# Optimization experiments

Hardware: AMD Instinct MI355X
Metric: run time of the kernel (lower is better)

The kernel has to match this reference:

```python
import jax, jax.numpy as jnp
import numpy as np

A, V, T = 32, 32, 128          # per-modality hidden dims
PF = 128                       # post_fusion_dim
FUSED = (A + 1) * (V + 1) * (T + 1)  # 140481
B = 256


def setup_inputs() -> dict:
    key = jax.random.key(0)
    ks = jax.random.split(key, 9)
    s1 = 1.0 / np.sqrt(FUSED)
    s2 = 1.0 / np.sqrt(PF)
    return {
        "audio_x": jax.random.normal(ks[0], (B, A), dtype=jnp.float32),
        "video_x": jax.random.normal(ks[1], (B, V), dtype=jnp.float32),
        "text_x": jax.random.normal(ks[2], (B, T), dtype=jnp.float32),
        "W1": jax.random.uniform(ks[3], (FUSED, PF), jnp.float32, -s1, s1),
        "b1": jax.random.uniform(ks[4], (PF,), jnp.float32, -s1, s1),
        "W2": jax.random.uniform(ks[5], (PF, PF), jnp.float32, -s2, s2),
        "b2": jax.random.uniform(ks[6], (PF,), jnp.float32, -s2, s2),
        "W3": jax.random.uniform(ks[7], (PF, 1), jnp.float32, -s2, s2),
        "b3": jax.random.uniform(ks[8], (1,), jnp.float32, -s2, s2),
    }


def reference(audio_x, video_x, text_x, W1, b1, W2, b2, W3, b3):
    b = audio_x.shape[0]
    ones = jnp.ones((b, 1), dtype=audio_x.dtype)
    a = jnp.concatenate([ones, audio_x], axis=1)  # (B, A+1)
    v = jnp.concatenate([ones, video_x], axis=1)  # (B, V+1)
    t = jnp.concatenate([ones, text_x], axis=1)   # (B, T+1)
    # trilinear outer product, flattened: (B, (A+1)*(V+1)*(T+1))
    fusion = jnp.einsum("ba,bv,bt->bavt", a, v, t).reshape(b, -1)
    h1 = jax.nn.relu(fusion @ W1 + b1)
    h2 = jax.nn.relu(h1 @ W2 + b2)
    return h2 @ W3 + b3
```

## Files before the change

kernel.cpp:

```cpp
#include <hip/hip_runtime.h>
#include <hip/hip_bf16.h>
#include <stdint.h>

#define BATCH 256
#define PFD 128
#define T1 129
#define NPAIRS 1089
#define BKSTR 72
#define CHUNK 8

typedef short bf16x8 __attribute__((ext_vector_type(8)));
typedef float f32x4 __attribute__((ext_vector_type(4)));

static __device__ __forceinline__ unsigned bits_of(float f){ union{float f;unsigned u;}x;x.f=f;return x.u; }
static __device__ __forceinline__ float float_of(unsigned u){ union{float f;unsigned u;}x;x.u=u;return x.f; }
static __device__ __forceinline__ unsigned pk_bf16(float a, float b){
  union { __hip_bfloat162 h; unsigned u; } c;
  c.h = __float22bfloat162_rn(make_float2(a, b));
  return c.u;
}

__global__ __launch_bounds__(512, 2) void tfn_k1(
    const float* __restrict__ audio, const float* __restrict__ video,
    const float* __restrict__ text, const float* __restrict__ W1,
    unsigned short* __restrict__ part, int S) {
  __shared__ __align__(16) short b_lds[2][PFD * BKSTR];
  __shared__ __align__(16) float av_lds[BATCH * CHUNK];

  const int tid = threadIdx.x;
  const int bk = blockIdx.x;
  const int npb = NPAIRS / S, rem0 = NPAIRS % S;
  const int p0 = bk * npb + (bk < rem0 ? bk : rem0);
  const int np = npb + (bk < rem0 ? 1 : 0);

  const int wave = tid >> 6, lane = tid & 63;
  const int l15 = lane & 15, quad = lane >> 4;
  const int sn = tid & 127, skg = tid >> 7;

  float treg[2][32];
  float t128r[2];
  #pragma unroll
  for (int mt = 0; mt < 2; ++mt) {
    const int m = wave * 32 + mt * 16 + l15;
    t128r[mt] = text[m * 128 + 127];
    #pragma unroll
    for (int ks = 0; ks < 4; ++ks)
      #pragma unroll
      for (int j = 0; j < 8; ++j) {
        const int it = ks * 32 + quad * 8 + j;
        treg[mt][ks * 8 + j] = (it == 0) ? 1.0f : text[m * 128 + it - 1];
      }
  }

  f32x4 acc[2][8];
  #pragma unroll
  for (int a = 0; a < 2; ++a)
    #pragma unroll
    for (int b = 0; b < 8; ++b) acc[a][b] = f32x4{0.f, 0.f, 0.f, 0.f};

  float pf0[16], pf1[16], rv[8];

  for (int c0 = 0; c0 < np; c0 += CHUNK) {
    const int nc = (np - c0) < CHUNK ? (np - c0) : CHUNK;
    const int pbase = p0 + c0;
    __syncthreads();
    if (tid < BATCH) {
      const int m = tid;
      for (int j = 0; j < nc; ++j) {
        int p = pbase + j;
        int ia = p / 33, iv = p - ia * 33;
        float a = (ia == 0) ? 1.0f : audio[m * 32 + ia - 1];
        float v = (iv == 0) ? 1.0f : video[m * 32 + iv - 1];
        av_lds[m * CHUNK + j] = a * v;
      }
    }
    #pragma unroll
    for (int j = 0; j < 8; ++j) {
      int kk = skg * 8 + j;
      rv[j] = (kk < nc) ? W1[((long)(pbase + kk) * T1 + 128) * PFD + sn] : 0.0f;
    }
    {
      const long rb = (long)pbase * T1;
      #pragma unroll
      for (int g = 0; g < 2; ++g)
        #pragma unroll
        for (int j = 0; j < 8; ++j) {
          pf0[g * 8 + j] = W1[(rb + g * 32 + skg * 8 + j) * PFD + sn];
          pf1[g * 8 + j] = W1[(rb + 64 + g * 32 + skg * 8 + j) * PFD + sn];
        }
    }
    for (int sp = 0; sp < nc; ++sp) {
      float avm[2];
      __syncthreads();
      avm[0] = av_lds[(wave * 32 + l15) * CHUNK + sp];
      avm[1] = av_lds[(wave * 32 + 16 + l15) * CHUNK + sp];
      {
        union { bf16x8 v; unsigned u[4]; } w0, w1;
        #pragma unroll
        for (int d = 0; d < 4; ++d) {
          w0.u[d] = pk_bf16(pf0[2 * d], pf0[2 * d + 1]);
          w1.u[d] = pk_bf16(pf0[8 + 2 * d], pf0[8 + 2 * d + 1]);
        }
        *(bf16x8*)&b_lds[0][sn * BKSTR + skg * 8] = w0.v;
        *(bf16x8*)&b_lds[0][sn * BKSTR + 32 + skg * 8] = w1.v;
      }
      if (sp + 1 < nc) {
        const long rb = (long)(pbase + sp + 1) * T1;
        #pragma unroll
        for (int g = 0; g < 2; ++g)
          #pragma unroll
          for (int j = 0; j < 8; ++j)
            pf0[g * 8 + j] = W1[(rb + g * 32 + skg * 8 + j) * PFD + sn];
      }
      __syncthreads();
      #pragma unroll
      for (int ks = 0; ks < 2; ++ks) {
        bf16x8 A0, A1;
        {
          union { bf16x8 v; unsigned u[4]; } c0u, c1u;
          #pragma unroll
          for (int d = 0; d < 4; ++d) {
            c0u.u[d] = pk_bf16(avm[0] * treg[0][ks * 8 + 2 * d], avm[0] * treg[0][ks * 8 + 2 * d + 1]);
            c1u.u[d] = pk_bf16(avm[1] * treg[1][ks * 8 + 2 * d], avm[1] * treg[1][ks * 8 + 2 * d + 1]);
          }
          A0 = c0u.v; A1 = c1u.v;
        }
        #pragma unroll
        for (int nt = 0; nt < 8; ++nt) {
          bf16x8 bf = *(const bf16x8*)&b_lds[0][(nt * 16 + l15) * BKSTR + ks * 32 + quad * 8];
          acc[0][nt] = __builtin_amdgcn_mfma_f32_16x16x32_bf16(A0, bf, acc[0][nt], 0, 0, 0);
          acc[1][nt] = __builtin_amdgcn_mfma_f32_16x16x32_bf16(A1, bf, acc[1][nt], 0, 0, 0);
        }
      }
      __syncthreads();
      {
        union { bf16x8 v; unsigned u[4]; } w0, w1;
        #pragma unroll
        for (int d = 0; d < 4; ++d) {
          w0.u[d] = pk_bf16(pf1[2 * d], pf1[2 * d + 1]);
          w1.u[d] = pk_bf16(pf1[8 + 2 * d], pf1[8 + 2 * d + 1]);
        }
        *(bf16x8*)&b_lds[1][sn * BKSTR + skg * 8] = w0.v;
        *(bf16x8*)&b_lds[1][sn * BKSTR + 32 + skg * 8] = w1.v;
      }
      if (sp + 1 < nc) {
        const long rb = (long)(pbase + sp + 1) * T1 + 64;
        #pragma unroll
        for (int g = 0; g < 2; ++g)
          #pragma unroll
          for (int j = 0; j < 8; ++j)
            pf1[g * 8 + j] = W1[(rb + g * 32 + skg * 8 + j) * PFD + sn];
      }
      __syncthreads();
      #pragma unroll
      for (int ks2 = 0; ks2 < 2; ++ks2) {
        const int ks = 2 + ks2;
        bf16x8 A0, A1;
        {
          union { bf16x8 v; unsigned u[4]; } c0u, c1u;
          #pragma unroll
          for (int d = 0; d < 4; ++d) {
            c0u.u[d] = pk_bf16(avm[0] * treg[0][ks * 8 + 2 * d], avm[0] * treg[0][ks * 8 + 2 * d + 1]);
            c1u.u[d] = pk_bf16(avm[1] * treg[1][ks * 8 + 2 * d], avm[1] * treg[1][ks * 8 + 2 * d + 1]);
          }
          A0 = c0u.v; A1 = c1u.v;
        }
        #pragma unroll
        for (int nt = 0; nt < 8; ++nt) {
          bf16x8 bf = *(const bf16x8*)&b_lds[1][(nt * 16 + l15) * BKSTR + ks2 * 32 + quad * 8];
          acc[0][nt] = __builtin_amdgcn_mfma_f32_16x16x32_bf16(A0, bf, acc[0][nt], 0, 0, 0);
          acc[1][nt] = __builtin_amdgcn_mfma_f32_16x16x32_bf16(A1, bf, acc[1][nt], 0, 0, 0);
        }
      }
    }
    __syncthreads();
    {
      union { bf16x8 v; unsigned u[4]; } w;
      #pragma unroll
      for (int d = 0; d < 4; ++d) w.u[d] = pk_bf16(rv[2 * d], rv[2 * d + 1]);
      *(bf16x8*)&b_lds[0][sn * BKSTR + skg * 8] = w.v;
    }
    __syncthreads();
    {
      bf16x8 A[2];
      #pragma unroll
      for (int mt = 0; mt < 2; ++mt) {
        const int m = wave * 32 + mt * 16 + l15;
        union { bf16x8 v; unsigned u[4]; } c;
        #pragma unroll
        for (int d = 0; d < 4; ++d) {
          int k0 = quad * 8 + 2 * d, k1 = k0 + 1;
          float f0 = (k0 < nc) ? av_lds[m * CHUNK + k0] * t128r[mt] : 0.0f;
          float f1 = (k1 < nc) ? av_lds[m * CHUNK + k1] * t128r[mt] : 0.0f;
          c.u[d] = pk_bf16(f0, f1);
        }
        A[mt] = c.v;
      }
      #pragma unroll
      for (int nt = 0; nt < 8; ++nt) {
        bf16x8 bf = *(const bf16x8*)&b_lds[0][(nt * 16 + l15) * BKSTR + quad * 8];
        acc[0][nt] = __builtin_amdgcn_mfma_f32_16x16x32_bf16(A[0], bf, acc[0][nt], 0, 0, 0);
        acc[1][nt] = __builtin_amdgcn_mfma_f32_16x16x32_bf16(A[1], bf, acc[1][nt], 0, 0, 0);
      }
    }
  }

  #pragma unroll
  for (int mt = 0; mt < 2; ++mt)
    #pragma unroll
    for (int r = 0; r < 4; ++r) {
      const int m = wave * 32 + mt * 16 + quad * 4 + r;
      union { bf16x8 v; unsigned u[4]; } w;
      #pragma unroll
      for (int d = 0; d < 4; ++d) w.u[d] = pk_bf16(acc[mt][2 * d][r], acc[mt][2 * d + 1][r]);
      *(bf16x8*)&part[((size_t)m * S + bk) * PFD + l15 * 8] = w.v;
    }
}

__global__ __launch_bounds__(1024) void tfn_k2(
    const unsigned short* __restrict__ part, const float* __restrict__ b1,
    const float* __restrict__ W2, const float* __restrict__ b2,
    const float* __restrict__ W3, const float* __restrict__ b3,
    float* __restrict__ out, int S) {
  __shared__ float sred[1024 * 4];
  __shared__ float h1s[PFD];
  __shared__ float a2s[1024];
  __shared__ float red[2];
  const int m = blockIdx.x, tid = threadIdx.x;
  const int g = tid & 31, q = tid >> 5;
  const unsigned short* base = part + (size_t)m * S * PFD;
  float s0 = 0, s1 = 0, s2 = 0, s3 = 0;
  for (int bkk = q; bkk < S; bkk += 32) {
    uint2 v = *(const uint2*)&base[(size_t)bkk * PFD + g * 4];
    s0 += float_of(v.x << 16);
    s1 += float_of(v.x & 0xFFFF0000u);
    s2 += float_of(v.y << 16);
    s3 += float_of(v.y & 0xFFFF0000u);
  }
  sred[tid * 4 + 0] = s0; sred[tid * 4 + 1] = s1;
  sred[tid * 4 + 2] = s2; sred[tid * 4 + 3] = s3;
  __syncthreads();
  if (tid < PFD) {
    const int p = tid;
    float h = 0;
    #pragma unroll
    for (int bl = 0; bl < 32; ++bl) h += sred[(bl * 32 + (p >> 2)) * 4 + (p & 3)];
    const int n = (p & 7) * 16 + (p >> 3);
    h1s[n] = fmaxf(h + b1[n], 0.0f);
  }
  __syncthreads();
  const int n = tid & 127, kq = tid >> 7;
  float a2 = 0.0f;
  const int k0 = kq * 16;
  #pragma unroll
  for (int k = 0; k < 16; ++k) a2 += h1s[k0 + k] * W2[(k0 + k) * PFD + n];
  a2s[tid] = a2;
  __syncthreads();
  if (tid < 128) {
    float h2 = 0.0f;
    #pragma unroll
    for (int j = 0; j < 8; ++j) h2 += a2s[n + 128 * j];
    h2 = fmaxf(h2 + b2[n], 0.0f);
    float pr = h2 * W3[n];
    #pragma unroll
    for (int off = 32; off > 0; off >>= 1) pr += __shfl_down(pr, off);
    if ((tid & 63) == 0) red[tid >> 6] = pr;
  }
  __syncthreads();
  if (tid == 0) out[m] = red[0] + red[1] + b3[0];
}

extern "C" void kernel_launch(void* const* d_in, const int* in_sizes, int n_in,
                              void* d_out, int out_size, void* d_ws, size_t ws_size,
                              hipStream_t stream) {
  const float* audio = (const float*)d_in[0];
  const float* video = (const float*)d_in[1];
  const float* text  = (const float*)d_in[2];
  const float* W1 = (const float*)d_in[3];
  const float* b1 = (const float*)d_in[4];
  const float* W2 = (const float*)d_in[5];
  const float* b2 = (const float*)d_in[6];
  const float* W3 = (const float*)d_in[7];
  const float* b3 = (const float*)d_in[8];
  unsigned short* part = (unsigned short*)d_ws;

  const size_t slab = (size_t)BATCH * PFD * sizeof(unsigned short);
  int S = (int)(ws_size / slab);
  if (S > 512) S = 512;
  if (S < 1) S = 1;

  tfn_k1<<<S, 512, 0, stream>>>(audio, video, text, W1, part, S);
  tfn_k2<<<BATCH, 1024, 0, stream>>>(part, b1, W2, b2, W3, b3, (float*)d_out, S);
}
```

Measured before the change: 145.3 us.

## Stage full K tile per pair in double-buffered LDS and cap grid at 256

The per-pair loop used to stage W1 in two 64-row halves, each with its own pair of barriers. It now converts all 128 rows of a pair into one of two LDS buffers chosen by pair parity. That cuts the barriers to one per pair and lets the next pair's global prefetch overlap the MFMA work. The LDS row stride grows to fit the full tile, which raises shared memory per block. The number of split-K blocks is also capped at 256 instead of 512, which shrinks the partial sums the second kernel must reduce but gives each block more pairs and fewer blocks per CU.

```diff
diff --git a/kernel.cpp b/kernel.cpp
--- a/kernel.cpp
+++ b/kernel.cpp
@@ -6,13 +6,12 @@
 #define PFD 128
 #define T1 129
 #define NPAIRS 1089
-#define BKSTR 72
+#define BK2 136
 #define CHUNK 8
 
 typedef short bf16x8 __attribute__((ext_vector_type(8)));
 typedef float f32x4 __attribute__((ext_vector_type(4)));
 
-static __device__ __forceinline__ unsigned bits_of(float f){ union{float f;unsigned u;}x;x.f=f;return x.u; }
 static __device__ __forceinline__ float float_of(unsigned u){ union{float f;unsigned u;}x;x.u=u;return x.f; }
 static __device__ __forceinline__ unsigned pk_bf16(float a, float b){
   union { __hip_bfloat162 h; unsigned u; } c;
@@ -24,7 +23,7 @@
     const float* __restrict__ audio, const float* __restrict__ video,
     const float* __restrict__ text, const float* __restrict__ W1,
     unsigned short* __restrict__ part, int S) {
-  __shared__ __align__(16) short b_lds[2][PFD * BKSTR];
+  __shared__ __align__(16) short b_lds[2][PFD * BK2];
   __shared__ __align__(16) float av_lds[BATCH * CHUNK];
 
   const int tid = threadIdx.x;
@@ -58,7 +57,7 @@
     #pragma unroll
     for (int b = 0; b < 8; ++b) acc[a][b] = f32x4{0.f, 0.f, 0.f, 0.f};
 
-  float pf0[16], pf1[16], rv[8];
+  float pf[32], rv[8];
 
   for (int c0 = 0; c0 < np; c0 += CHUNK) {
     const int nc = (np - c0) < CHUNK ? (np - c0) : CHUNK;
@@ -82,92 +81,48 @@
     {
       const long rb = (long)pbase * T1;
       #pragma unroll
-      for (int g = 0; g < 2; ++g)
-        #pragma unroll
-        for (int j = 0; j < 8; ++j) {
-          pf0[g * 8 + j] = W1[(rb + g * 32 + skg * 8 + j) * PFD + sn];
-          pf1[g * 8 + j] = W1[(rb + 64 + g * 32 + skg * 8 + j) * PFD + sn];
-        }
+      for (int g = 0; g < 4; ++g)
+        #pragma unroll
+        for (int j = 0; j < 8; ++j)
+          pf[g * 8 + j] = W1[(rb + g * 32 + skg * 8 + j) * PFD + sn];
     }
     for (int sp = 0; sp < nc; ++sp) {
-      float avm[2];
+      {
+        union { bf16x8 v; unsigned u[4]; } w;
+        #pragma unroll
+        for (int g = 0; g < 4; ++g) {
+          #pragma unroll
+          for (int d = 0; d < 4; ++d)
+            w.u[d] = pk_bf16(pf[g * 8 + 2 * d], pf[g * 8 + 2 * d + 1]);
+          *(bf16x8*)&b_lds[sp & 1][sn * BK2 + g * 32 + skg * 8] = w.v;
+        }
+      }
       __syncthreads();
-      avm[0] = av_lds[(wave * 32 + l15) * CHUNK + sp];
-      avm[1] = av_lds[(wave * 32 + 16 + l15) * CHUNK + sp];
-      {
-        union { bf16x8 v; unsigned u[4]; } w0, w1;
-        #pragma unroll
-        for (int d = 0; d < 4; ++d) {
-          w0.u[d] = pk_bf16(pf0[2 * d], pf0[2 * d + 1]);
-          w1.u[d] = pk_bf16(pf0[8 + 2 * d], pf0[8 + 2 * d + 1]);
-        }
-        *(bf16x8*)&b_lds[0][sn * BKSTR + skg * 8] = w0.v;
-        *(bf16x8*)&b_lds[0][sn * BKSTR + 32 + skg * 8] = w1.v;
-      }
       if (sp + 1 < nc) {
         const long rb = (long)(pbase + sp + 1) * T1;
         #pragma unroll
-        for (int g = 0; g < 2; ++g)
+        for (int g = 0; g < 4; ++g)
           #pragma unroll
           for (int j = 0; j < 8; ++j)
-            pf0[g * 8 + j] = W1[(rb + g * 32 + skg * 8 + j) * PFD + sn];
-      }
-      __syncthreads();
-      #pragma unroll
-      for (int ks = 0; ks < 2; ++ks) {
+            pf[g * 8 + j] = W1[(rb + g * 32 + skg * 8 + j) * PFD + sn];
+      }
+      const float avm0 = av_lds[(wave * 32 + l15) * CHUNK + sp];
+      const float avm1 = av_lds[(wave * 32 + 16 + l15) * CHUNK + sp];
+      #pragma unroll
+      for (int ks = 0; ks < 4; ++ks) {
         bf16x8 A0, A1;
         {
           union { bf16x8 v; unsigned u[4]; } c0u, c1u;
           #pragma unroll
           for (int d = 0; d < 4; ++d) {
-            c0u.u[d] = pk_bf16(avm[0] * treg[0][ks * 8 + 2 * d], avm[0] * treg[0][ks * 8 + 2 * d + 1]);
-            c1u.u[d] = pk_bf16(avm[1] * treg[1][ks * 8 + 2 * d], avm[1] * treg[1][ks * 8 + 2 * d + 1]);
+            c0u.u[d] = pk_bf16(avm0 * treg[0][ks * 8 + 2 * d], avm0 * treg[0][ks * 8 + 2 * d + 1]);
+            c1u.u[d] = pk_bf16(avm1 * treg[1][ks * 8 + 2 * d], avm1 * treg[1][ks * 8 + 2 * d + 1]);
           }
           A0 = c0u.v; A1 = c1u.v;
         }
         #pragma unroll
         for (int nt = 0; nt < 8; ++nt) {
-          bf16x8 bf = *(const bf16x8*)&b_lds[0][(nt * 16 + l15) * BKSTR + ks * 32 + quad * 8];
-          acc[0][nt] = __builtin_amdgcn_mfma_f32_16x16x32_bf16(A0, bf, acc[0][nt], 0, 0, 0);
-          acc[1][nt] = __builtin_amdgcn_mfma_f32_16x16x32_bf16(A1, bf, acc[1][nt], 0, 0, 0);
-        }
-      }
-      __syncthreads();
-      {
-        union { bf16x8 v; unsigned u[4]; } w0, w1;
-        #pragma unroll
-        for (int d = 0; d < 4; ++d) {
-          w0.u[d] = pk_bf16(pf1[2 * d], pf1[2 * d + 1]);
-          w1.u[d] = pk_bf16(pf1[8 + 2 * d], pf1[8 + 2 * d + 1]);
-        }
-        *(bf16x8*)&b_lds[1][sn * BKSTR + skg * 8] = w0.v;
-        *(bf16x8*)&b_lds[1][sn * BKSTR + 32 + skg * 8] = w1.v;
-      }
-      if (sp + 1 < nc) {
-        const long rb = (long)(pbase + sp + 1) * T1 + 64;
-        #pragma unroll
-        for (int g = 0; g < 2; ++g)
-          #pragma unroll
-          for (int j = 0; j < 8; ++j)
-            pf1[g * 8 + j] = W1[(rb + g * 32 + skg * 8 + j) * PFD + sn];
-      }
-      __syncthreads();
-      #pragma unroll
-      for (int ks2 = 0; ks2 < 2; ++ks2) {
-        const int ks = 2 + ks2;
-        bf16x8 A0, A1;
-        {
-          union { bf16x8 v; unsigned u[4]; } c0u, c1u;
-          #pragma unroll
-          for (int d = 0; d < 4; ++d) {
-            c0u.u[d] = pk_bf16(avm[0] * treg[0][ks * 8 + 2 * d], avm[0] * treg[0][ks * 8 + 2 * d + 1]);
-            c1u.u[d] = pk_bf16(avm[1] * treg[1][ks * 8 + 2 * d], avm[1] * treg[1][ks * 8 + 2 * d + 1]);
-          }
-          A0 = c0u.v; A1 = c1u.v;
-        }
-        #pragma unroll
-        for (int nt = 0; nt < 8; ++nt) {
-          bf16x8 bf = *(const bf16x8*)&b_lds[1][(nt * 16 + l15) * BKSTR + ks2 * 32 + quad * 8];
+          bf16x8 bf = *(const bf16x8*)&b_lds[sp & 1][(nt * 16 + l15) * BK2 + ks * 32 + quad * 8];
           acc[0][nt] = __builtin_amdgcn_mfma_f32_16x16x32_bf16(A0, bf, acc[0][nt], 0, 0, 0);
           acc[1][nt] = __builtin_amdgcn_mfma_f32_16x16x32_bf16(A1, bf, acc[1][nt], 0, 0, 0);
         }
@@ -178,7 +133,7 @@
       union { bf16x8 v; unsigned u[4]; } w;
       #pragma unroll
       for (int d = 0; d < 4; ++d) w.u[d] = pk_bf16(rv[2 * d], rv[2 * d + 1]);
-      *(bf16x8*)&b_lds[0][sn * BKSTR + skg * 8] = w.v;
+      *(bf16x8*)&b_lds[0][sn * BK2 + skg * 8] = w.v;
     }
     __syncthreads();
     {
@@ -198,7 +153,7 @@
       }
       #pragma unroll
       for (int nt = 0; nt < 8; ++nt) {
-        bf16x8 bf = *(const bf16x8*)&b_lds[0][(nt * 16 + l15) * BKSTR + quad * 8];
+        bf16x8 bf = *(const bf16x8*)&b_lds[0][(nt * 16 + l15) * BK2 + quad * 8];
         acc[0][nt] = __builtin_amdgcn_mfma_f32_16x16x32_bf16(A[0], bf, acc[0][nt], 0, 0, 0);
         acc[1][nt] = __builtin_amdgcn_mfma_f32_16x16x32_bf16(A[1], bf, acc[1][nt], 0, 0, 0);
       }
@@ -286,7 +241,7 @@
 
   const size_t slab = (size_t)BATCH * PFD * sizeof(unsigned short);
   int S = (int)(ws_size / slab);
-  if (S > 512) S = 512;
+  if (S > 256) S = 256;
   if (S < 1) S = 1;
 
   tfn_k1<<<S, 512, 0, stream>>>(audio, video, text, W1, part, S);
```

Result: faster. 135.9 us (median of 2 runs) (-6.5%).
